# Optimization experiments

Measured on AMD Instinct MI355X. Metric: run time of the kernel, lower is better.

The kernel has to match this reference:

```python
import jax, jax.numpy as jnp
import numpy as np

B, T, S, H, D = 2, 2048, 2048, 16, 64
E = H * D  # embed_dim = 1024


def setup_inputs() -> dict:
    key = jax.random.key(0)
    k1, k2, k3, k4 = jax.random.split(key, 4)
    q = jax.random.normal(k1, (B, T, H, D), jnp.float32)
    kv = jax.random.normal(k2, (B, S, 2, H, D), jnp.float32)
    # nn.MultiheadAttention packed in-projection (xavier-ish scale) and out-projection
    in_proj_w = jax.random.normal(k3, (3 * E, E), jnp.float32) * (1.0 / np.sqrt(E)).astype(np.float32)
    in_proj_b = jnp.zeros((3 * E,), jnp.float32)
    out_proj_w = jax.random.normal(k4, (E, E), jnp.float32) * (1.0 / np.sqrt(E)).astype(np.float32)
    out_proj_b = jnp.zeros((E,), jnp.float32)
    return {"q": q, "kv": kv, "in_proj_w": in_proj_w, "in_proj_b": in_proj_b,
            "out_proj_w": out_proj_w, "out_proj_b": out_proj_b}


def reference(q, kv, in_proj_w, in_proj_b, out_proj_w, out_proj_b):
    Bq, Tq, Hh, Dd = q.shape
    Ss = kv.shape[1]
    Ee = Hh * Dd
    # flatten heads: q -> (B,T,E); kv unbinds k (two=0) and v (two=1)
    qf = q.reshape(Bq, Tq, Ee)
    kf = kv[:, :, 0].reshape(Bq, Ss, Ee)
    vf = kv[:, :, 1].reshape(Bq, Ss, Ee)
    wq, wk, wv = jnp.split(in_proj_w, 3, axis=0)
    bq, bk, bv = jnp.split(in_proj_b, 3)
    qp = (qf @ wq.T + bq).reshape(Bq, Tq, Hh, Dd).transpose(0, 2, 1, 3)  # bhtd
    kp = (kf @ wk.T + bk).reshape(Bq, Ss, Hh, Dd).transpose(0, 2, 1, 3)  # bhsd
    vp = (vf @ wv.T + bv).reshape(Bq, Ss, Hh, Dd).transpose(0, 2, 1, 3)  # bhsd
    scale = 1.0 / jnp.sqrt(jnp.asarray(Dd, qp.dtype))
    scores = jnp.einsum('bhtd,bhsd->bhts', qp, kp) * scale
    attn = jax.nn.softmax(scores, axis=-1)  # full SxS materialization, as in non-fused MHA
    ctx = jnp.einsum('bhts,bhsd->bhtd', attn, vp)
    ctx = ctx.transpose(0, 2, 1, 3).reshape(Bq, Tq, Ee)
    out = (ctx @ out_proj_w.T + out_proj_b).reshape(Bq, Tq, Hh, Dd)
    # need_weights=True default: weights averaged over heads -> (B,T,S)
    attn_weights = attn.mean(axis=1)
    return out, attn_weights
```

## Files before the change

### kernel.cpp

```cpp
#include <hip/hip_runtime.h>
#include <math.h>

#define Bb 2
#define Tt 2048
#define Ssz 2048
#define Hh 16
#define Dd 64
#define Ee 1024

#define NQ  (Bb*Tt*Ee)
#define NKV (Bb*Ssz*Ee)
#define NW  (3*Ee*Ee)
#define NWO (Ee*Ee)

#define LOG2E 1.44269504088896f

typedef __bf16 bf16x8 __attribute__((ext_vector_type(8)));
typedef float  floatx4 __attribute__((ext_vector_type(4)));
typedef unsigned short u16;
typedef unsigned int   u32;

__device__ __forceinline__ u16 f2bf(float f) {
    __bf16 h = (__bf16)f;
    union { __bf16 h; u16 u; } v; v.h = h; return v.u;
}
__device__ __forceinline__ float bf2f(u16 b) {
    union { u32 u; float f; } v; v.u = ((u32)b) << 16; return v.f;
}
__device__ __forceinline__ float load_f(const void* p, int i, bool isbf) {
    if (isbf) return bf2f(((const u16*)p)[i]);
    return ((const float*)p)[i];
}
__device__ __forceinline__ u32 load2(const void* p, int i, bool isbf) {
    if (isbf) return ((const u32*)p)[i >> 1];
    float2 f = ((const float2*)p)[i >> 1];
    return (u32)f2bf(f.x) | ((u32)f2bf(f.y) << 16);
}

typedef __attribute__((address_space(1))) const unsigned int gas_u32;
typedef __attribute__((address_space(3))) unsigned int las_u32;
__device__ __forceinline__ void gl_lds16(const u16* g, u16* l) {
    __builtin_amdgcn_global_load_lds((gas_u32*)g, (las_u32*)l, 16, 0, 0);
}

__device__ __forceinline__ int swz(int k, int row) {
    return (k & ~63) | ((((k >> 3) ^ row) & 7) << 3) | (k & 7);
}

__global__ void k_detect(const u32* __restrict__ qw, int* __restrict__ flag) {
    __shared__ int cnt;
    if (threadIdx.x == 0) cnt = 0;
    __syncthreads();
    int h = 0;
    for (int i = threadIdx.x; i < 4096; i += 256) {
        u32 w = qw[i];
        u32 b = (w >> 8) & 0x7Fu;
        if ((b & 0x7Cu) == 0x3Cu) h++;
    }
    atomicAdd(&cnt, h);
    __syncthreads();
    if (threadIdx.x == 0) flag[0] = (cnt > 2048) ? 1 : 0;
}

__global__ void k_pack(const void* __restrict__ q, const void* __restrict__ kv,
                       const void* __restrict__ w_in, const void* __restrict__ b_in,
                       const void* __restrict__ w_out, const void* __restrict__ b_out,
                       const int* __restrict__ flag,
                       u32* __restrict__ qb, u32* __restrict__ kb, u32* __restrict__ vb,
                       u32* __restrict__ wb, u32* __restrict__ wob, float* __restrict__ biases) {
    bool isbf = flag[0] != 0;
    int i = (blockIdx.x * 256 + threadIdx.x) * 2;
    if (i < NQ) { int row = i >> 10, k = i & 1023;
        qb[(((size_t)row << 10) | (u32)swz(k, row)) >> 1] = load2(q, i, isbf); return; }
    i -= NQ;
    if (i < NKV) { int row = i >> 10, e = i & 1023;
        kb[(((size_t)row << 10) | (u32)swz(e, row)) >> 1] = load2(kv, row*2048 + e, isbf); return; }
    i -= NKV;
    if (i < NKV) { int row = i >> 10, e = i & 1023;
        vb[(((size_t)row << 10) | (u32)swz(e, row)) >> 1] = load2(kv, row*2048 + 1024 + e, isbf); return; }
    i -= NKV;
    if (i < NW) { int row = i >> 10, k = i & 1023;
        wb[(((size_t)row << 10) | (u32)swz(k, row)) >> 1] = load2(w_in, i, isbf); return; }
    i -= NW;
    if (i < NWO) { int row = i >> 10, k = i & 1023;
        wob[(((size_t)row << 10) | (u32)swz(k, row)) >> 1] = load2(w_out, i, isbf); return; }
    i -= NWO;
    if (i < 3072) { biases[i] = load_f(b_in, i, isbf); biases[i+1] = load_f(b_in, i+1, isbf); return; }
    i -= 3072;
    if (i < 1024) { biases[3072+i] = load_f(b_out, i, isbf); biases[3072+i+1] = load_f(b_out, i+1, isbf); }
}

__device__ __forceinline__ void gemm128(const u16* __restrict__ Ab, const u16* __restrict__ Wb,
                                        u16* As, u16* Ws, floatx4 (&acc)[4][4], int tid) {
    int lane = tid & 63, w = tid >> 6, q = lane >> 4, ml = lane & 15;
    int mh = (w >> 1) * 64, nh = (w & 1) * 64;
    int rs = tid >> 3, cs = (tid & 7) * 8;
    for (int k0 = 0; k0 < 1024; k0 += 64) {
        __syncthreads();
#pragma unroll
        for (int j = 0; j < 4; ++j)
            gl_lds16(Ab + (size_t)(j*32 + rs) * 1024 + k0 + cs, &As[(j*32 + rs)*64 + cs]);
#pragma unroll
        for (int j = 0; j < 4; ++j)
            gl_lds16(Wb + (size_t)(j*32 + rs) * 1024 + k0 + cs, &Ws[(j*32 + rs)*64 + cs]);
        __syncthreads();
#pragma unroll
        for (int kk = 0; kk < 2; ++kk) {
            int gs = (((kk*4 + q) ^ ml) & 7) * 8;
            bf16x8 af[4], bfv[4];
#pragma unroll
            for (int mt = 0; mt < 4; ++mt) af[mt]  = *(const bf16x8*)&As[(mh + mt*16 + ml)*64 + gs];
#pragma unroll
            for (int nt = 0; nt < 4; ++nt) bfv[nt] = *(const bf16x8*)&Ws[(nh + nt*16 + ml)*64 + gs];
#pragma unroll
            for (int mt = 0; mt < 4; ++mt)
#pragma unroll
                for (int nt = 0; nt < 4; ++nt)
                    acc[mt][nt] = __builtin_amdgcn_mfma_f32_16x16x32_bf16(af[mt], bfv[nt], acc[mt][nt], 0, 0, 0);
        }
    }
}

__global__ __launch_bounds__(256) void k_gemm_qkv(const u16* __restrict__ qb, const u16* __restrict__ kb,
                                                  const u16* __restrict__ vb, const u16* __restrict__ wb,
                                                  const float* __restrict__ biases,
                                                  u16* __restrict__ Qp, u16* __restrict__ Kp,
                                                  u16* __restrict__ Vt) {
    __shared__ u16 As[128 * 64];
    __shared__ u16 Ws[128 * 64];
    int mode = blockIdx.z;
    const u16* A = (mode == 0) ? qb : (mode == 1) ? kb : vb;
    const u16* W = wb + (size_t)mode * Ee * Ee;
    const float* bias = biases + mode * 1024;
    int n0 = blockIdx.x * 128, m0 = blockIdx.y * 128;
    int tid = threadIdx.x, lane = tid & 63;
    int w = tid >> 6, q = lane >> 4, ml = lane & 15;
    int mh = (w >> 1) * 64, nh = (w & 1) * 64;

    floatx4 acc[4][4];
#pragma unroll
    for (int a = 0; a < 4; ++a)
#pragma unroll
        for (int b2 = 0; b2 < 4; ++b2) acc[a][b2] = (floatx4){0.f, 0.f, 0.f, 0.f};

    gemm128(A + (size_t)m0 * 1024, W + (size_t)n0 * 1024, As, Ws, acc, tid);

#pragma unroll
    for (int mt = 0; mt < 4; ++mt) {
#pragma unroll
        for (int nt = 0; nt < 4; ++nt) {
#pragma unroll
            for (int rg = 0; rg < 4; ++rg) {
                int m = m0 + mh + mt*16 + q*4 + rg;
                int n = n0 + nh + nt*16 + ml;
                float val = acc[mt][nt][rg] + bias[n];
                int b = m >> 11, t = m & 2047, hh = n >> 6, d = n & 63;
                if (mode == 0) {
                    int dsw = ((((d >> 3) ^ t) & 7) << 3) | (d & 7);
                    Qp[((size_t)(b*16 + hh) * 2048 + t) * 64 + dsw] = f2bf(val * (0.125f * LOG2E));
                } else if (mode == 1) {
                    int dsw = ((((d >> 3) ^ t) & 7) << 3) | (d & 7);
                    Kp[((size_t)(b*16 + hh) * 2048 + t) * 64 + dsw] = f2bf(val);
                } else {
                    int tsw = (t & ~63) | ((((t >> 3) ^ d) & 7) << 3) | (t & 7);
                    Vt[((size_t)(b*16 + hh) * 64 + d) * 2048 + tsw] = f2bf(val);
                }
            }
        }
    }
}

__global__ __launch_bounds__(256) void k_gemm_out(const u16* __restrict__ A, const u16* __restrict__ W,
                                                  const float* __restrict__ bias, void* __restrict__ Cout,
                                                  const int* __restrict__ flag) {
    __shared__ u16 As[128 * 64];
    __shared__ u16 Ws[128 * 64];
    int n0 = blockIdx.x * 128, m0 = blockIdx.y * 128;
    int tid = threadIdx.x, lane = tid & 63;
    int w = tid >> 6, q = lane >> 4, ml = lane & 15;
    int mh = (w >> 1) * 64, nh = (w & 1) * 64;

    floatx4 acc[4][4];
#pragma unroll
    for (int a = 0; a < 4; ++a)
#pragma unroll
        for (int b2 = 0; b2 < 4; ++b2) acc[a][b2] = (floatx4){0.f, 0.f, 0.f, 0.f};

    gemm128(A + (size_t)m0 * 1024, W + (size_t)n0 * 1024, As, Ws, acc, tid);

    bool outbf = flag[0] != 0;
#pragma unroll
    for (int mt = 0; mt < 4; ++mt) {
#pragma unroll
        for (int nt = 0; nt < 4; ++nt) {
#pragma unroll
            for (int rg = 0; rg < 4; ++rg) {
                int m = m0 + mh + mt*16 + q*4 + rg;
                int n = n0 + nh + nt*16 + ml;
                float val = acc[mt][nt][rg] + bias[n];
                if (outbf) ((u16*)Cout)[(size_t)m * 1024 + n] = f2bf(val);
                else       ((float*)Cout)[(size_t)m * 1024 + n] = val;
            }
        }
    }
}

__global__ __launch_bounds__(512) void k_flash(const u16* __restrict__ Qp, const u16* __restrict__ Kp,
                                               const u16* __restrict__ Vt, u16* __restrict__ ctx,
                                               float* __restrict__ lbuf) {
    __shared__ u16 Qs[128 * 64];
    __shared__ u16 Ks[2][64 * 64];
    __shared__ u16 Vs[2][64 * 64];
    __shared__ u16 Ps[128 * 64];
    int t0 = blockIdx.x * 128;
    int h  = blockIdx.y;
    int b  = blockIdx.z;
    const u16* Qh = Qp + (size_t)(b*16 + h) * 2048 * 64;
    const u16* Kh = Kp + (size_t)(b*16 + h) * 2048 * 64;
    const u16* Vh = Vt + (size_t)(b*16 + h) * 64 * 2048;
    int tid = threadIdx.x, lane = tid & 63;
    int w = tid >> 6, q = lane >> 4, ml = lane & 15;
    int rsw = tid >> 3, cs = (tid & 7) * 8;

#pragma unroll
    for (int j = 0; j < 2; ++j)
        gl_lds16(Qh + (size_t)(t0 + j*64 + rsw) * 64 + cs, &Qs[(j*64 + rsw)*64 + cs]);
    gl_lds16(Kh + (size_t)rsw * 64 + cs, &Ks[0][rsw*64 + cs]);
    gl_lds16(Vh + (size_t)rsw * 2048 + cs, &Vs[0][rsw*64 + cs]);
    __syncthreads();

    bf16x8 qf[2];
#pragma unroll
    for (int kk = 0; kk < 2; ++kk)
        qf[kk] = *(const bf16x8*)&Qs[(w*16 + ml)*64 + (((kk*4 + q) ^ ml) & 7)*8];

    float lp[4] = {0.f, 0.f, 0.f, 0.f};
    floatx4 ct[4];
#pragma unroll
    for (int i = 0; i < 4; ++i) ct[i] = (floatx4){0.f, 0.f, 0.f, 0.f};

    int cur = 0;
    for (int s0 = 0; s0 < 2048; s0 += 64) {
        if (s0 + 64 < 2048) {
            gl_lds16(Kh + (size_t)(s0 + 64 + rsw) * 64 + cs, &Ks[cur ^ 1][rsw*64 + cs]);
            gl_lds16(Vh + (size_t)rsw * 2048 + (s0 + 64) + cs, &Vs[cur ^ 1][rsw*64 + cs]);
        }
        const u16* Ksc = Ks[cur];
        const u16* Vsc = Vs[cur];

        floatx4 sc[4];
#pragma unroll
        for (int i = 0; i < 4; ++i) sc[i] = (floatx4){0.f, 0.f, 0.f, 0.f};
#pragma unroll
        for (int kk = 0; kk < 2; ++kk) {
            int gs = (((kk*4 + q) ^ ml) & 7) * 8;
#pragma unroll
            for (int nt = 0; nt < 4; ++nt) {
                bf16x8 kf = *(const bf16x8*)&Ksc[(nt*16 + ml)*64 + gs];
                sc[nt] = __builtin_amdgcn_mfma_f32_16x16x32_bf16(qf[kk], kf, sc[nt], 0, 0, 0);
            }
        }

#pragma unroll
        for (int nt = 0; nt < 4; ++nt) {
#pragma unroll
            for (int rg = 0; rg < 4; ++rg) {
                float p = __builtin_amdgcn_exp2f(sc[nt][rg]);
                lp[rg] += p;
                int rr = q*4 + rg;
                Ps[(w*16 + rr)*64 + (((nt*2 + (ml >> 3)) ^ rr) & 7)*8 + (ml & 7)] = f2bf(p);
            }
        }

#pragma unroll
        for (int kk = 0; kk < 2; ++kk) {
            int gs = (((kk*4 + q) ^ ml) & 7) * 8;
            bf16x8 pf = *(const bf16x8*)&Ps[(w*16 + ml)*64 + gs];
#pragma unroll
            for (int nt = 0; nt < 4; ++nt) {
                bf16x8 vf = *(const bf16x8*)&Vsc[(nt*16 + ml)*64 + gs];
                ct[nt] = __builtin_amdgcn_mfma_f32_16x16x32_bf16(pf, vf, ct[nt], 0, 0, 0);
            }
        }

        __syncthreads();
        cur ^= 1;
    }

#pragma unroll
    for (int rg = 0; rg < 4; ++rg)
#pragma unroll
        for (int off = 1; off < 16; off <<= 1) lp[rg] += __shfl_xor(lp[rg], off, 16);
    if (ml == 0) {
        size_t base = (size_t)(b*16 + h) * 2048 + t0 + w*16 + q*4;
#pragma unroll
        for (int rg = 0; rg < 4; ++rg) lbuf[base + rg] = lp[rg];
    }

    float il[4];
#pragma unroll
    for (int rg = 0; rg < 4; ++rg) il[rg] = 1.f / lp[rg];
#pragma unroll
    for (int nt = 0; nt < 4; ++nt) {
#pragma unroll
        for (int rg = 0; rg < 4; ++rg) {
            int t = t0 + w*16 + q*4 + rg;
            int c64 = nt*16 + ml;
            int col = h*64 + (((((c64 >> 3) ^ t) & 7)) << 3) + (c64 & 7);
            ctx[(size_t)(b*2048 + t) * 1024 + col] = f2bf(ct[nt][rg] * il[rg]);
        }
    }
}

__global__ __launch_bounds__(256) void k_attnw(const u16* __restrict__ Qp, const u16* __restrict__ Kp,
                                               const float* __restrict__ lbuf,
                                               void* __restrict__ dout, const int* __restrict__ flag) {
    __shared__ u16 Qs[64 * 64];
    __shared__ u16 Ks[128 * 64];
    int s0 = blockIdx.x * 128;
    int t0 = blockIdx.y * 64;
    int b  = blockIdx.z;
    int tid = threadIdx.x, lane = tid & 63;
    int w = tid >> 6, q = lane >> 4, ml = lane & 15;
    int rsw = tid >> 3, cs = (tid & 7) * 8;

    floatx4 aw[8];
#pragma unroll
    for (int i = 0; i < 8; ++i) aw[i] = (floatx4){0.f, 0.f, 0.f, 0.f};

    for (int h = 0; h < 16; ++h) {
        const u16* Qh = Qp + (size_t)(b*16 + h) * 2048 * 64;
        const u16* Kh = Kp + (size_t)(b*16 + h) * 2048 * 64;
        __syncthreads();
#pragma unroll
        for (int j = 0; j < 2; ++j)
            gl_lds16(Qh + (size_t)(t0 + j*32 + rsw) * 64 + cs, &Qs[(j*32 + rsw)*64 + cs]);
#pragma unroll
        for (int j = 0; j < 4; ++j)
            gl_lds16(Kh + (size_t)(s0 + j*32 + rsw) * 64 + cs, &Ks[(j*32 + rsw)*64 + cs]);
        __syncthreads();

        float il[4];
        size_t sb = (size_t)(b*16 + h) * 2048 + t0 + w*16 + q*4;
#pragma unroll
        for (int rg = 0; rg < 4; ++rg) il[rg] = 1.f / lbuf[sb + rg];

        floatx4 sc[8];
#pragma unroll
        for (int i = 0; i < 8; ++i) sc[i] = (floatx4){0.f, 0.f, 0.f, 0.f};
#pragma unroll
        for (int kk = 0; kk < 2; ++kk) {
            int gs = (((kk*4 + q) ^ ml) & 7) * 8;
            bf16x8 qfr = *(const bf16x8*)&Qs[(w*16 + ml)*64 + gs];
#pragma unroll
            for (int nt = 0; nt < 8; ++nt) {
                bf16x8 kfr = *(const bf16x8*)&Ks[(nt*16 + ml)*64 + gs];
                sc[nt] = __builtin_amdgcn_mfma_f32_16x16x32_bf16(qfr, kfr, sc[nt], 0, 0, 0);
            }
        }
#pragma unroll
        for (int nt = 0; nt < 8; ++nt)
#pragma unroll
            for (int rg = 0; rg < 4; ++rg)
                aw[nt][rg] += __builtin_amdgcn_exp2f(sc[nt][rg]) * il[rg];
    }

    bool outbf = flag[0] != 0;
    const size_t attn_base = (size_t)Bb * Tt * Ee;
#pragma unroll
    for (int nt = 0; nt < 8; ++nt) {
#pragma unroll
        for (int rg = 0; rg < 4; ++rg) {
            int t = t0 + w*16 + q*4 + rg;
            int s = s0 + nt*16 + ml;
            float val = aw[nt][rg] * 0.0625f;
            size_t idx = attn_base + (size_t)(b*2048 + t) * 2048 + s;
            if (outbf) ((u16*)dout)[idx] = f2bf(val);
            else       ((float*)dout)[idx] = val;
        }
    }
}

extern "C" void kernel_launch(void* const* d_in, const int* in_sizes, int n_in,
                              void* d_out, int out_size, void* d_ws, size_t ws_size,
                              hipStream_t stream) {
    const void* q     = d_in[0];
    const void* kv    = d_in[1];
    const void* w_in  = d_in[2];
    const void* b_in  = d_in[3];
    const void* w_out = d_in[4];
    const void* b_out = d_in[5];

    char* ws = (char*)d_ws;
    size_t off = 0;
    auto alloc = [&](size_t bytes) -> void* {
        void* p = ws + off;
        off += (bytes + 255) & ~(size_t)255;
        return p;
    };
    int*   flag   = (int*)alloc(256);
    u16*   qb     = (u16*)alloc((size_t)NQ * 2);
    u16*   kb     = (u16*)alloc((size_t)NKV * 2);
    u16*   vb     = (u16*)alloc((size_t)NKV * 2);
    u16*   wb     = (u16*)alloc((size_t)NW * 2);
    u16*   wob    = (u16*)alloc((size_t)NWO * 2);
    float* biases = (float*)alloc(4096 * 4);
    u16*   Qp     = (u16*)alloc((size_t)NQ * 2);
    u16*   Kp     = (u16*)alloc((size_t)NKV * 2);
    u16*   Vt     = (u16*)alloc((size_t)NKV * 2);
    u16*   ctx    = (u16*)alloc((size_t)NQ * 2);
    float* lbuf   = (float*)alloc((size_t)Bb * Hh * Tt * 4);

    k_detect<<<1, 256, 0, stream>>>((const u32*)q, flag);

    int totalPairs = (NQ + NKV + NKV + NW + NWO + 4096) / 2;
    k_pack<<<(totalPairs + 255) / 256, 256, 0, stream>>>(q, kv, w_in, b_in, w_out, b_out, flag,
                                                         (u32*)qb, (u32*)kb, (u32*)vb,
                                                         (u32*)wb, (u32*)wob, biases);

    k_gemm_qkv<<<dim3(8, 32, 3), 256, 0, stream>>>(qb, kb, vb, wb, biases, Qp, Kp, Vt);

    k_flash<<<dim3(Tt / 128, Hh, Bb), 512, 0, stream>>>(Qp, Kp, Vt, ctx, lbuf);
    k_attnw<<<dim3(Ssz / 128, Tt / 64, Bb), 256, 0, stream>>>(Qp, Kp, lbuf, d_out, flag);

    k_gemm_out<<<dim3(8, 32), 256, 0, stream>>>(ctx, wob, biases + 3072, d_out, flag);
}
```

Before: 289.3 us.

## Keep softmax probabilities in registers via transposed QK MFMA layout

Swaps the MFMA operands so the score tile comes out transposed, letting each lane's exp'd probabilities act directly as the A operand of 16x16x16 bf16 MFMAs for the PV product. This removes the shared-memory P buffer, its scattered writes and reads, and shrinks LDS use. The row sums now reduce across the quad groups with two shuffles, followed by a shuffle to redistribute the inverse. The trade-off is twice as many smaller MFMAs and narrower 8-byte V reads.

```diff
diff --git a/kernel.cpp b/kernel.cpp
--- a/kernel.cpp
+++ b/kernel.cpp
@@ -17,6 +17,7 @@
 
 typedef __bf16 bf16x8 __attribute__((ext_vector_type(8)));
 typedef float  floatx4 __attribute__((ext_vector_type(4)));
+typedef short  short4_ __attribute__((ext_vector_type(4)));
 typedef unsigned short u16;
 typedef unsigned int   u32;
 
@@ -211,7 +212,6 @@
     __shared__ u16 Qs[128 * 64];
     __shared__ u16 Ks[2][64 * 64];
     __shared__ u16 Vs[2][64 * 64];
-    __shared__ u16 Ps[128 * 64];
     int t0 = blockIdx.x * 128;
     int h  = blockIdx.y;
     int b  = blockIdx.z;
@@ -234,7 +234,7 @@
     for (int kk = 0; kk < 2; ++kk)
         qf[kk] = *(const bf16x8*)&Qs[(w*16 + ml)*64 + (((kk*4 + q) ^ ml) & 7)*8];
 
-    float lp[4] = {0.f, 0.f, 0.f, 0.f};
+    float lp = 0.f;
     floatx4 ct[4];
 #pragma unroll
     for (int i = 0; i < 4; ++i) ct[i] = (floatx4){0.f, 0.f, 0.f, 0.f};
@@ -257,29 +257,28 @@
 #pragma unroll
             for (int nt = 0; nt < 4; ++nt) {
                 bf16x8 kf = *(const bf16x8*)&Ksc[(nt*16 + ml)*64 + gs];
-                sc[nt] = __builtin_amdgcn_mfma_f32_16x16x32_bf16(qf[kk], kf, sc[nt], 0, 0, 0);
-            }
-        }
-
+                sc[nt] = __builtin_amdgcn_mfma_f32_16x16x32_bf16(kf, qf[kk], sc[nt], 0, 0, 0);
+            }
+        }
+
+        short4_ pa[4];
 #pragma unroll
         for (int nt = 0; nt < 4; ++nt) {
 #pragma unroll
             for (int rg = 0; rg < 4; ++rg) {
                 float p = __builtin_amdgcn_exp2f(sc[nt][rg]);
-                lp[rg] += p;
-                int rr = q*4 + rg;
-                Ps[(w*16 + rr)*64 + (((nt*2 + (ml >> 3)) ^ rr) & 7)*8 + (ml & 7)] = f2bf(p);
-            }
-        }
-
-#pragma unroll
-        for (int kk = 0; kk < 2; ++kk) {
-            int gs = (((kk*4 + q) ^ ml) & 7) * 8;
-            bf16x8 pf = *(const bf16x8*)&Ps[(w*16 + ml)*64 + gs];
+                lp += p;
+                pa[nt][rg] = (short)f2bf(p);
+            }
+        }
+
+#pragma unroll
+        for (int ks = 0; ks < 4; ++ks) {
 #pragma unroll
             for (int nt = 0; nt < 4; ++nt) {
-                bf16x8 vf = *(const bf16x8*)&Vsc[(nt*16 + ml)*64 + gs];
-                ct[nt] = __builtin_amdgcn_mfma_f32_16x16x32_bf16(pf, vf, ct[nt], 0, 0, 0);
+                const u16* vp = &Vsc[(nt*16 + ml)*64 + ((((ks*2 + (q >> 1)) ^ ml) & 7) << 3) + (q & 1)*4];
+                short4_ vf = *(const short4_*)vp;
+                ct[nt] = __builtin_amdgcn_mfma_f32_16x16x16bf16_1k(pa[ks], vf, ct[nt], 0, 0, 0);
             }
         }
 
@@ -287,19 +286,16 @@
         cur ^= 1;
     }
 
-#pragma unroll
-    for (int rg = 0; rg < 4; ++rg)
-#pragma unroll
-        for (int off = 1; off < 16; off <<= 1) lp[rg] += __shfl_xor(lp[rg], off, 16);
-    if (ml == 0) {
-        size_t base = (size_t)(b*16 + h) * 2048 + t0 + w*16 + q*4;
-#pragma unroll
-        for (int rg = 0; rg < 4; ++rg) lbuf[base + rg] = lp[rg];
+    lp += __shfl_xor(lp, 16);
+    lp += __shfl_xor(lp, 32);
+    if (lane < 16) {
+        lbuf[(size_t)(b*16 + h) * 2048 + t0 + w*16 + ml] = lp;
     }
 
     float il[4];
 #pragma unroll
-    for (int rg = 0; rg < 4; ++rg) il[rg] = 1.f / lp[rg];
+    for (int rg = 0; rg < 4; ++rg) il[rg] = 1.f / __shfl(lp, q*4 + rg);
+
 #pragma unroll
     for (int nt = 0; nt < 4; ++nt) {
 #pragma unroll
```

Result: no change. 288.2 us (-0.4%).
